# Optimization experiments

Measured on AMD Instinct MI355X. Metric: run time of the kernel, lower is better.

Reference implementation:

```python
import jax, jax.numpy as jnp
import numpy as np

N, E, D, H, K = 100000, 1600000, 512, 256, 64


def setup_inputs() -> dict:
    key = jax.random.key(0)
    ks = jax.random.split(key, 8)
    x = jax.random.normal(ks[0], (N, D), dtype=jnp.float32)
    edge_index = jax.random.randint(ks[1], (2, E), 0, N, dtype=jnp.int64)
    W1 = jax.random.normal(ks[2], (D, H), dtype=jnp.float32) / np.sqrt(D)
    b1 = jnp.zeros((H,), dtype=jnp.float32)
    W2 = jax.random.normal(ks[3], (H, H), dtype=jnp.float32) / np.sqrt(H)
    b2 = jnp.zeros((H,), dtype=jnp.float32)
    Wk = jax.random.normal(ks[4], (H, K), dtype=jnp.float32) / np.sqrt(H)
    log_tau = jnp.array(np.log(1.0), dtype=jnp.float32)
    return {"x": x, "edge_index": edge_index, "W1": W1, "b1": b1,
            "W2": W2, "b2": b2, "Wk": Wk, "log_tau": log_tau}


def _gcn_norm(edge_index, n):
    # add self-loops, compute sym-normalized edge weights (PyG GCNConv default)
    loop = jnp.arange(n, dtype=edge_index.dtype)
    src = jnp.concatenate([edge_index[0], loop])
    dst = jnp.concatenate([edge_index[1], loop])
    deg = jax.ops.segment_sum(jnp.ones_like(dst, dtype=jnp.float32), dst, num_segments=n)
    dinv = jnp.where(deg > 0, jax.lax.rsqrt(deg), 0.0)
    norm = dinv[src] * dinv[dst]  # [E+N]
    return src, dst, norm


def _gcn_conv(h, W, b, src, dst, norm, n):
    hw = h @ W                      # dense GEMM [n, out]
    msg = hw[src] * norm[:, None]   # gather + scale
    out = jax.ops.segment_sum(msg, dst, num_segments=n)  # scatter-add
    return out + b


def reference(x, edge_index, W1, b1, W2, b2, Wk, log_tau):
    n = x.shape[0]
    src, dst, norm = _gcn_norm(edge_index, n)
    h = jax.nn.relu(_gcn_conv(x, W1, b1, src, dst, norm, n))
    h = _gcn_conv(h, W2, b2, src, dst, norm, n)
    logits = h @ Wk                 # [n, K]
    tau = jnp.exp(log_tau)
    S = jax.nn.softmax(logits / tau, axis=-1)
    return (S, logits)
```

## Files before the change

kernel.cpp:

```cpp
#include <hip/hip_runtime.h>

typedef unsigned short u16;
typedef unsigned int u32;

__device__ __forceinline__ float bfl(u32 u) { union { u32 i; float f; } v; v.i = u << 16; return v.f; }
__device__ __forceinline__ float bfh(u32 u) { union { u32 i; float f; } v; v.i = u & 0xffff0000u; return v.f; }
__device__ __forceinline__ float bf2f(u16 u) { union { u32 i; float f; } v; v.i = ((u32)u) << 16; return v.f; }
__device__ __forceinline__ u16 f2bf(float f) {
    union { float f; u32 i; } v; v.f = f;
    u32 r = v.i + 0x7fffu + ((v.i >> 16) & 1u);
    return (u16)(r >> 16);
}

typedef const __attribute__((address_space(1))) unsigned int* gas_u32;
typedef __attribute__((address_space(3))) unsigned int* las_u32;
__device__ __forceinline__ void async_cp16(const void* g, void* l) {
    __builtin_amdgcn_global_load_lds((gas_u32)g, (las_u32)l, 16, 0, 0);
}

__global__ void k_detect(const u32* __restrict__ xw, const int* __restrict__ eiw,
                         const void* __restrict__ ltau, int* __restrict__ flags,
                         int* __restrict__ bcount,
                         int xwords, int E, int nb) {
    __shared__ int cf32, ci64nz;
    if (threadIdx.x == 0) { cf32 = 0; ci64nz = 0; }
    __syncthreads();
    int t = threadIdx.x;
    for (int i = t; i < nb; i += 256) bcount[i] = 0;
    int xs = xwords / 256;
    u32 w = xw[(size_t)t * xs];
    int e = (int)((w >> 23) & 0xFFu);
    if (e >= 100 && e <= 140) atomicAdd(&cf32, 1);
    int es = E / 256;
    int hw = eiw[2 * (size_t)t * es + 1];
    if (hw != 0) atomicAdd(&ci64nz, 1);
    __syncthreads();
    if (t == 0) {
        int f32 = (cf32 >= 192) ? 1 : 0;
        flags[0] = f32;
        flags[1] = (ci64nz == 0) ? 1 : 0;
        ((float*)flags)[2] = f32 ? ((const float*)ltau)[0] : bf2f(((const u16*)ltau)[0]);
    }
}

__global__ __launch_bounds__(256) void k_edges_count(const int* __restrict__ ei,
                                                     int* __restrict__ src, int* __restrict__ dst,
                                                     int* __restrict__ bcount,
                                                     int e, int nb, const int* __restrict__ flags) {
    __shared__ int h[1024];
    int t = threadIdx.x;
    for (int i = t; i < nb; i += 256) h[i] = 0;
    __syncthreads();
    const int i64 = flags[1];
    int chunk = (e + gridDim.x - 1) / gridDim.x;
    int beg = blockIdx.x * chunk;
    int end = beg + chunk; if (end > e) end = e;
    for (int i = beg + t; i < end; i += 256) {
        int s, d;
        if (i64) { s = ei[2 * i]; d = ei[2 * (e + i)]; }
        else     { s = ei[i];     d = ei[e + i]; }
        src[i] = s; dst[i] = d;
        atomicAdd(&h[d >> 7], 1);
    }
    __syncthreads();
    for (int i = t; i < nb; i += 256) { int v = h[i]; if (v) atomicAdd(&bcount[i], v); }
}

__global__ __launch_bounds__(1024) void k_bscan(const int* __restrict__ bcount, int* __restrict__ bbase,
                                                int* __restrict__ bcursor, int nb) {
    int t = threadIdx.x;
    int per = (nb + 1023) >> 10;
    int b0 = t * per;
    int ls[8];
    int s = 0;
#pragma unroll
    for (int j = 0; j < 8; j++) {
        int v = 0;
        if (j < per && b0 + j < nb) v = bcount[b0 + j];
        ls[j] = v; s += v;
    }
    int lane = t & 63, w = t >> 6;
    int inc = s;
    for (int d = 1; d < 64; d <<= 1) { int u = __shfl_up(inc, d); if (lane >= d) inc += u; }
    __shared__ int wsum[16];
    __shared__ int gtot;
    if (lane == 63) wsum[w] = inc;
    __syncthreads();
    if (t == 0) { int a = 0; for (int i = 0; i < 16; i++) { int x = wsum[i]; wsum[i] = a; a += x; } gtot = a; }
    __syncthreads();
    int base = wsum[w] + inc - s;
#pragma unroll
    for (int j = 0; j < 8; j++) {
        if (j < per && b0 + j < nb) { bbase[b0 + j] = base; bcursor[b0 + j] = base; base += ls[j]; }
    }
    if (t == 0) bbase[nb] = gtot;
}

__global__ __launch_bounds__(256) void k_bscatter(const int* __restrict__ src, const int* __restrict__ dst,
                                                  int* __restrict__ bcursor, u32* __restrict__ ebuf,
                                                  int e, int nb) {
    __shared__ int h[1024];
    __shared__ int lbase[1024];
    int t = threadIdx.x;
    for (int i = t; i < nb; i += 256) h[i] = 0;
    __syncthreads();
    int chunk = (e + gridDim.x - 1) / gridDim.x;
    int beg = blockIdx.x * chunk;
    int end = beg + chunk; if (end > e) end = e;
    for (int i = beg + t; i < end; i += 256) atomicAdd(&h[dst[i] >> 7], 1);
    __syncthreads();
    for (int i = t; i < nb; i += 256) {
        int v = h[i];
        lbase[i] = v ? atomicAdd(&bcursor[i], v) : 0;
        h[i] = 0;
    }
    __syncthreads();
    for (int i = beg + t; i < end; i += 256) {
        int d = dst[i];
        int b = d >> 7;
        int p = lbase[b] + atomicAdd(&h[b], 1);
        ebuf[p] = ((u32)(d & 127) << 25) | (u32)src[i];
    }
}

__global__ __launch_bounds__(256) void k_bcsr(const u32* __restrict__ ebuf, const int* __restrict__ bbase,
                                              int* __restrict__ row_ptr, float* __restrict__ dinv,
                                              int* __restrict__ col, int n, int nb, int e) {
    __shared__ int hist[128], sc[128], cur[128];
    int b = blockIdx.x, t = threadIdx.x;
    if (t < 128) hist[t] = 0;
    __syncthreads();
    int beg = bbase[b], end = bbase[b + 1];
    for (int j = beg + t; j < end; j += 256) atomicAdd(&hist[ebuf[j] >> 25], 1);
    __syncthreads();
    if (t < 128) sc[t] = hist[t];
    __syncthreads();
    for (int d = 1; d < 128; d <<= 1) {
        int v = 0;
        if (t < 128 && t >= d) v = sc[t - d];
        __syncthreads();
        if (t < 128) sc[t] += v;
        __syncthreads();
    }
    if (t < 128) {
        int node = (b << 7) + t;
        if (node < n) {
            int ex = sc[t] - hist[t];
            row_ptr[node] = beg + ex;
            dinv[node] = rsqrtf((float)(hist[t] + 1));
            cur[t] = ex;
        }
    }
    if (b == 0 && t == 0) row_ptr[n] = e;
    __syncthreads();
    for (int j = beg + t; j < end; j += 256) {
        u32 ev = ebuf[j];
        int dl = (int)(ev >> 25);
        int p = atomicAdd(&cur[dl], 1);
        col[beg + p] = (int)(ev & 0x1FFFFFFu);
    }
}

__global__ void k_transpose_flex(const void* __restrict__ in, u16* __restrict__ out,
                                 int R, int C, const int* __restrict__ flags) {
    int idx = blockIdx.x * 256 + threadIdx.x;
    if (idx >= R * C) return;
    u16 v = flags[0] ? f2bf(((const float*)in)[idx]) : ((const u16*)in)[idx];
    int r = idx / C, c = idx % C;
    out[(size_t)c * R + r] = v;
}

typedef __bf16 bf16x8 __attribute__((ext_vector_type(8)));
typedef float floatx4 __attribute__((ext_vector_type(4)));

template <int WROWS, int WCOLS, int TM, int TN, int MODE, bool AFLEX, bool OFLEX>
__global__ __launch_bounds__(WROWS * WCOLS * 64, 4)
void k_gemm_bt(const void* __restrict__ A,
               const u16* __restrict__ Bt,
               void* __restrict__ C,
               const float* __restrict__ dinv,
               const int* __restrict__ flags,
               long long obase,
               int M, int Nd, int Kd) {
    constexpr int THREADS = WROWS * WCOLS * 64;
    constexpr int BM = WROWS * TM * 16;
    constexpr int BN = WCOLS * TN * 16;
    constexpr int BK = 32;
    __shared__ u16 As[2][BM][BK];
    __shared__ u16 Bs[2][BN][BK];
    const int af32 = AFLEX ? flags[0] : 0;
    const int of32 = OFLEX ? flags[0] : 0;
    const int tid = threadIdx.x;
    const int m0 = blockIdx.y * BM;
    const int n0 = blockIdx.x * BN;
    const int lane = tid & 63;
    const int wave = tid >> 6;
    const int wm = wave / WCOLS;
    const int wn = wave % WCOLS;
    const int mrow = lane & 15;
    const int quad = lane >> 4;

    floatx4 acc[TM][TN];
#pragma unroll
    for (int i = 0; i < TM; i++)
#pragma unroll
        for (int j = 0; j < TN; j++) { floatx4 z = {0.f, 0.f, 0.f, 0.f}; acc[i][j] = z; }

    auto stage = [&](int kk, int buf) {
        if (AFLEX && af32) {
#pragma unroll
            for (int idx = tid * 8; idx < BM * BK; idx += THREADS * 8) {
                int r = idx >> 5, k = idx & 31;
                int gr = m0 + r;
                u16 t8[8] = {0, 0, 0, 0, 0, 0, 0, 0};
                if (gr < M) {
                    const float* ap = (const float*)A + (size_t)gr * Kd + kk + k;
                    float4 f0 = *(const float4*)ap;
                    float4 f1 = *(const float4*)(ap + 4);
                    t8[0] = f2bf(f0.x); t8[1] = f2bf(f0.y); t8[2] = f2bf(f0.z); t8[3] = f2bf(f0.w);
                    t8[4] = f2bf(f1.x); t8[5] = f2bf(f1.y); t8[6] = f2bf(f1.z); t8[7] = f2bf(f1.w);
                }
                *(int4*)&As[buf][r][k] = *(const int4*)t8;
            }
#pragma unroll
            for (int idx = tid * 8; idx < BN * BK; idx += THREADS * 8) {
                int r = idx >> 5, k = idx & 31;
                int4 v = *(const int4*)(Bt + (size_t)(n0 + r) * Kd + kk + k);
                *(int4*)&Bs[buf][r][k] = v;
            }
        } else {
#pragma unroll
            for (int idx = tid * 8; idx < BM * BK; idx += THREADS * 8) {
                int r = idx >> 5, k = idx & 31;
                int gr = m0 + r;
                if (gr >= M) gr = M - 1;
                async_cp16((const u16*)A + (size_t)gr * Kd + kk + k, &As[buf][r][k]);
            }
#pragma unroll
            for (int idx = tid * 8; idx < BN * BK; idx += THREADS * 8) {
                int r = idx >> 5, k = idx & 31;
                async_cp16(Bt + (size_t)(n0 + r) * Kd + kk + k, &Bs[buf][r][k]);
            }
        }
    };

    const int steps = Kd / BK;
    stage(0, 0);
    for (int s = 0; s < steps; s++) {
        __syncthreads();
        if (s + 1 < steps) stage((s + 1) * BK, (s + 1) & 1);
        const int b = s & 1;
        bf16x8 af[TM], bfr[TN];
#pragma unroll
        for (int i = 0; i < TM; i++)
            af[i] = *(const bf16x8*)&As[b][wm * TM * 16 + i * 16 + mrow][quad * 8];
#pragma unroll
        for (int j = 0; j < TN; j++)
            bfr[j] = *(const bf16x8*)&Bs[b][wn * TN * 16 + j * 16 + mrow][quad * 8];
#pragma unroll
        for (int i = 0; i < TM; i++)
#pragma unroll
            for (int j = 0; j < TN; j++)
                acc[i][j] = __builtin_amdgcn_mfma_f32_16x16x32_bf16(af[i], bfr[j], acc[i][j], 0, 0, 0);
    }

#pragma unroll
    for (int i = 0; i < TM; i++) {
#pragma unroll
        for (int r = 0; r < 4; r++) {
            int grow = m0 + wm * TM * 16 + i * 16 + quad * 4 + r;
            if (grow < M) {
                float scale = (MODE == 0) ? dinv[grow] : 1.0f;
#pragma unroll
                for (int j = 0; j < TN; j++) {
                    int gcol = n0 + wn * TN * 16 + j * 16 + mrow;
                    float val = acc[i][j][r] * scale;
                    long long cidx = obase + (long long)grow * Nd + gcol;
                    if (OFLEX && of32) ((float*)C)[cidx] = val;
                    else               ((u16*)C)[cidx] = f2bf(val);
                }
            }
        }
    }
}

__global__ __launch_bounds__(256) void k_agg(const u16* __restrict__ g, u16* __restrict__ out,
                                             const int* __restrict__ row_ptr,
                                             const int* __restrict__ col,
                                             const float* __restrict__ dinv,
                                             const void* __restrict__ bias,
                                             const int* __restrict__ flags,
                                             int n, int do_relu) {
    int wid = (int)((blockIdx.x * 256 + threadIdx.x) >> 6);
    int lane = threadIdx.x & 63;
    if (wid >= n) return;
    int half = lane >> 5;
    int l = lane & 31;
    const u16* gp = g + (size_t)l * 8;
    float a0 = 0.f, a1 = 0.f, a2 = 0.f, a3 = 0.f, a4 = 0.f, a5 = 0.f, a6 = 0.f, a7 = 0.f;
    if (half == 0) {
        uint4 rv = *(const uint4*)(gp + (size_t)wid * 256);
        a0 += bfl(rv.x); a1 += bfh(rv.x); a2 += bfl(rv.y); a3 += bfh(rv.y);
        a4 += bfl(rv.z); a5 += bfh(rv.z); a6 += bfl(rv.w); a7 += bfh(rv.w);
    }
    int beg = row_ptr[wid], end = row_ptr[wid + 1];
    for (int base = beg; base < end; base += 64) {
        int m = end - base; if (m > 64) m = 64;
        int ci = (base + lane < end) ? col[base + lane] : 0;
        int j = 0;
        for (; j + 16 <= m; j += 16) {
            uint4 v[8];
#pragma unroll
            for (int q = 0; q < 8; q++) {
                int s = __shfl(ci, j + 2 * q + half);
                v[q] = *(const uint4*)(gp + (size_t)s * 256);
            }
#pragma unroll
            for (int q = 0; q < 8; q++) {
                a0 += bfl(v[q].x); a1 += bfh(v[q].x);
                a2 += bfl(v[q].y); a3 += bfh(v[q].y);
                a4 += bfl(v[q].z); a5 += bfh(v[q].z);
                a6 += bfl(v[q].w); a7 += bfh(v[q].w);
            }
        }
        for (; j < m; j += 2) {
            int idx = j + half;
            int s = __shfl(ci, idx < m ? idx : j);
            uint4 v = *(const uint4*)(gp + (size_t)s * 256);
            if (idx < m) {
                a0 += bfl(v.x); a1 += bfh(v.x); a2 += bfl(v.y); a3 += bfh(v.y);
                a4 += bfl(v.z); a5 += bfh(v.z); a6 += bfl(v.w); a7 += bfh(v.w);
            }
        }
    }
    a0 += __shfl_xor(a0, 32); a1 += __shfl_xor(a1, 32);
    a2 += __shfl_xor(a2, 32); a3 += __shfl_xor(a3, 32);
    a4 += __shfl_xor(a4, 32); a5 += __shfl_xor(a5, 32);
    a6 += __shfl_xor(a6, 32); a7 += __shfl_xor(a7, 32);
    if (half == 0) {
        float dv = dinv[wid];
        float b0, b1, b2, b3, b4, b5, b6, b7;
        if (flags[0]) {
            const float4* bp = (const float4*)bias;
            float4 q0 = bp[2 * l], q1 = bp[2 * l + 1];
            b0 = q0.x; b1 = q0.y; b2 = q0.z; b3 = q0.w;
            b4 = q1.x; b5 = q1.y; b6 = q1.z; b7 = q1.w;
        } else {
            uint4 bv = ((const uint4*)bias)[l];
            b0 = bfl(bv.x); b1 = bfh(bv.x); b2 = bfl(bv.y); b3 = bfh(bv.y);
            b4 = bfl(bv.z); b5 = bfh(bv.z); b6 = bfl(bv.w); b7 = bfh(bv.w);
        }
        a0 = a0 * dv + b0; a1 = a1 * dv + b1; a2 = a2 * dv + b2; a3 = a3 * dv + b3;
        a4 = a4 * dv + b4; a5 = a5 * dv + b5; a6 = a6 * dv + b6; a7 = a7 * dv + b7;
        if (do_relu) {
            a0 = fmaxf(a0, 0.f); a1 = fmaxf(a1, 0.f); a2 = fmaxf(a2, 0.f); a3 = fmaxf(a3, 0.f);
            a4 = fmaxf(a4, 0.f); a5 = fmaxf(a5, 0.f); a6 = fmaxf(a6, 0.f); a7 = fmaxf(a7, 0.f);
        }
        uint4 o;
        o.x = (u32)f2bf(a0) | ((u32)f2bf(a1) << 16);
        o.y = (u32)f2bf(a2) | ((u32)f2bf(a3) << 16);
        o.z = (u32)f2bf(a4) | ((u32)f2bf(a5) << 16);
        o.w = (u32)f2bf(a6) | ((u32)f2bf(a7) << 16);
        *(uint4*)(out + (size_t)wid * 256 + (size_t)l * 8) = o;
    }
}

__global__ __launch_bounds__(256) void k_softmax(void* __restrict__ out, long long NK,
                                                 const int* __restrict__ flags, int n) {
    int wid = (int)((blockIdx.x * 256 + threadIdx.x) >> 6);
    int lane = threadIdx.x & 63;
    if (wid >= n) return;
    int f32o = flags[0];
    float lt = ((const float*)flags)[2];
    float inv_tau = __expf(-lt);
    long long li = NK + (long long)wid * 64 + lane;
    float x = f32o ? ((const float*)out)[li] : bf2f(((const u16*)out)[li]);
    x *= inv_tau;
    float m = x;
    for (int d = 32; d; d >>= 1) m = fmaxf(m, __shfl_xor(m, d));
    float e = __expf(x - m);
    float s = e;
    for (int d = 32; d; d >>= 1) s += __shfl_xor(s, d);
    float r = e / s;
    long long si = (long long)wid * 64 + lane;
    if (f32o) ((float*)out)[si] = r;
    else      ((u16*)out)[si] = f2bf(r);
}

extern "C" void kernel_launch(void* const* d_in, const int* in_sizes, int n_in,
                              void* d_out, int out_size, void* d_ws, size_t ws_size,
                              hipStream_t stream) {
    const void* x    = d_in[0];
    const int*  ei   = (const int*)d_in[1];
    const void* W1   = d_in[2];
    const void* b1   = d_in[3];
    const void* W2   = d_in[4];
    const void* b2   = d_in[5];
    const void* Wk   = d_in[6];
    const void* ltau = d_in[7];
    const int D = 512, H = 256, K = 64;
    const int N = in_sizes[0] / D;
    const int E = in_sizes[1] / 2;
    const long long NK = (long long)N * K;
    const int nb = (N + 127) >> 7;

    u16* g = (u16*)d_ws;
    u16* h = g + (size_t)N * H;
    int* flags = (int*)(h + (size_t)N * H);
    int* srcv = (int*)g;
    int* dstv = srcv + E;
    u32* ebuf = (u32*)(dstv + E);

    size_t ooff = 0;
    auto oalloc = [&](size_t bytes) -> char* {
        char* p = (char*)d_out + ooff;
        ooff += (bytes + 255) & ~(size_t)255;
        return p;
    };
    int*   col     = (int*)oalloc((size_t)E * 4);
    float* dinv    = (float*)oalloc((size_t)N * 4);
    int*   row_ptr = (int*)oalloc((size_t)(N + 1) * 4);
    int*   bcount  = (int*)oalloc((size_t)nb * 4);
    int*   bbase   = (int*)oalloc((size_t)(nb + 1) * 4);
    int*   bcursor = (int*)oalloc((size_t)nb * 4);
    u16*   W1t     = (u16*)oalloc((size_t)D * H * 2);
    u16*   W2t     = (u16*)oalloc((size_t)H * H * 2);
    u16*   Wkt     = (u16*)oalloc((size_t)H * K * 2);

    auto g256 = [](long long n) { return (int)((n + 255) / 256); };

    k_detect<<<1, 256, 0, stream>>>((const u32*)x, ei, ltau, flags, bcount, in_sizes[0] / 2, E, nb);
    k_edges_count<<<256, 256, 0, stream>>>(ei, srcv, dstv, bcount, E, nb, flags);
    k_bscan<<<1, 1024, 0, stream>>>(bcount, bbase, bcursor, nb);
    k_bscatter<<<256, 256, 0, stream>>>(srcv, dstv, bcursor, ebuf, E, nb);
    k_bcsr<<<nb, 256, 0, stream>>>(ebuf, bbase, row_ptr, dinv, col, N, nb, E);

    k_transpose_flex<<<g256((long long)D * H), 256, 0, stream>>>(W1, W1t, D, H, flags);
    k_transpose_flex<<<g256((long long)H * H), 256, 0, stream>>>(W2, W2t, H, H, flags);
    k_transpose_flex<<<g256((long long)H * K), 256, 0, stream>>>(Wk, Wkt, H, K, flags);

    const int m64 = (N + 63) / 64;
    k_gemm_bt<1, 4, 4, 4, 0, true, false>
        <<<dim3(1, m64), 256, 0, stream>>>(x, W1t, g, dinv, flags, 0, N, H, D);
    k_agg<<<g256((long long)N * 64), 256, 0, stream>>>(g, h, row_ptr, col, dinv, b1, flags, N, 1);
    k_gemm_bt<1, 4, 4, 4, 0, false, false>
        <<<dim3(1, m64), 256, 0, stream>>>(h, W2t, g, dinv, flags, 0, N, H, H);
    k_agg<<<g256((long long)N * 64), 256, 0, stream>>>(g, h, row_ptr, col, dinv, b2, flags, N, 0);
    k_gemm_bt<1, 4, 4, 1, 1, false, true>
        <<<dim3(1, m64), 256, 0, stream>>>(h, Wkt, d_out, dinv, flags, NK, N, K, H);
    k_softmax<<<g256((long long)N * 64), 256, 0, stream>>>(d_out, NK, flags, N);
}
```

Before: 716.5 us.

## Fuse softmax into logits GEMM, batch rows per wave in aggregation, pack bf16 conversion

The final logits GEMM now stages its output tile in shared memory and computes the temperature softmax in the epilogue, so the separate softmax kernel and its reread of the logits go away. The aggregation kernel processes four rows per wave and loads the bias once per wave rather than once per row, with a quarter of the launched waves. The fp32-to-bf16 conversion in the first GEMM uses a packed hardware convert instruction. Scratch arrays move from the output buffer to the workspace. The trade-offs are less parallelism in aggregation and extra LDS traffic and syncs in the GEMM epilogue.

```diff
diff --git a/kernel.cpp b/kernel.cpp
--- a/kernel.cpp
+++ b/kernel.cpp
@@ -10,6 +10,11 @@
     union { float f; u32 i; } v; v.f = f;
     u32 r = v.i + 0x7fffu + ((v.i >> 16) & 1u);
     return (u16)(r >> 16);
+}
+__device__ __forceinline__ u32 pk2bf(float lo, float hi) {
+    u32 r;
+    asm("v_cvt_pk_bf16_f32 %0, %1, %2" : "=v"(r) : "v"(lo), "v"(hi));
+    return r;
 }
 
 typedef const __attribute__((address_space(1))) unsigned int* gas_u32;
@@ -186,8 +191,9 @@
     constexpr int BM = WROWS * TM * 16;
     constexpr int BN = WCOLS * TN * 16;
     constexpr int BK = 32;
-    __shared__ u16 As[2][BM][BK];
-    __shared__ u16 Bs[2][BN][BK];
+    __shared__ u16 SMEM[2 * (BM + BN) * BK];
+    auto As = (u16(*)[BM][BK])SMEM;
+    auto Bs = (u16(*)[BN][BK])(SMEM + 2 * BM * BK);
     const int af32 = AFLEX ? flags[0] : 0;
     const int of32 = OFLEX ? flags[0] : 0;
     const int tid = threadIdx.x;
@@ -212,15 +218,15 @@
             for (int idx = tid * 8; idx < BM * BK; idx += THREADS * 8) {
                 int r = idx >> 5, k = idx & 31;
                 int gr = m0 + r;
-                u16 t8[8] = {0, 0, 0, 0, 0, 0, 0, 0};
+                u32 t4[4] = {0, 0, 0, 0};
                 if (gr < M) {
                     const float* ap = (const float*)A + (size_t)gr * Kd + kk + k;
                     float4 f0 = *(const float4*)ap;
                     float4 f1 = *(const float4*)(ap + 4);
-                    t8[0] = f2bf(f0.x); t8[1] = f2bf(f0.y); t8[2] = f2bf(f0.z); t8[3] = f2bf(f0.w);
-                    t8[4] = f2bf(f1.x); t8[5] = f2bf(f1.y); t8[6] = f2bf(f1.z); t8[7] = f2bf(f1.w);
+                    t4[0] = pk2bf(f0.x, f0.y); t4[1] = pk2bf(f0.z, f0.w);
+                    t4[2] = pk2bf(f1.x, f1.y); t4[3] = pk2bf(f1.z, f1.w);
                 }
-                *(int4*)&As[buf][r][k] = *(const int4*)t8;
+                *(int4*)&As[buf][r][k] = *(const int4*)t4;
             }
 #pragma unroll
             for (int idx = tid * 8; idx < BN * BK; idx += THREADS * 8) {
@@ -264,6 +270,38 @@
                 acc[i][j] = __builtin_amdgcn_mfma_f32_16x16x32_bf16(af[i], bfr[j], acc[i][j], 0, 0, 0);
     }
 
+    if (MODE == 2) {
+        float inv_tau = __expf(-((const float*)flags)[2]);
+        float* Ct = (float*)SMEM;
+        __syncthreads();
+#pragma unroll
+        for (int i = 0; i < TM; i++)
+#pragma unroll
+            for (int r = 0; r < 4; r++) {
+                int row = i * 16 + quad * 4 + r;
+                Ct[row * 64 + wn * 16 + mrow] = acc[i][0][r];
+            }
+        __syncthreads();
+        for (int r16 = 0; r16 < 16; r16++) {
+            int row = r16 * 4 + wave;
+            float raw = Ct[row * 64 + lane];
+            float xv = raw * inv_tau;
+            float mx = xv;
+            for (int d = 32; d; d >>= 1) mx = fmaxf(mx, __shfl_xor(mx, d));
+            float ev = __expf(xv - mx);
+            float sm = ev;
+            for (int d = 32; d; d >>= 1) sm += __shfl_xor(sm, d);
+            float rr = ev / sm;
+            long long grow = m0 + row;
+            if (grow < M) {
+                long long si = grow * 64 + lane;
+                if (of32) { ((float*)C)[si] = rr; ((float*)C)[obase + si] = raw; }
+                else      { ((u16*)C)[si] = f2bf(rr); ((u16*)C)[obase + si] = f2bf(raw); }
+            }
+        }
+        return;
+    }
+
 #pragma unroll
     for (int i = 0; i < TM; i++) {
 #pragma unroll
@@ -291,100 +329,80 @@
                                              const void* __restrict__ bias,
                                              const int* __restrict__ flags,
                                              int n, int do_relu) {
-    int wid = (int)((blockIdx.x * 256 + threadIdx.x) >> 6);
+    int gw = (int)((blockIdx.x * 256 + threadIdx.x) >> 6);
     int lane = threadIdx.x & 63;
-    if (wid >= n) return;
     int half = lane >> 5;
     int l = lane & 31;
     const u16* gp = g + (size_t)l * 8;
-    float a0 = 0.f, a1 = 0.f, a2 = 0.f, a3 = 0.f, a4 = 0.f, a5 = 0.f, a6 = 0.f, a7 = 0.f;
-    if (half == 0) {
-        uint4 rv = *(const uint4*)(gp + (size_t)wid * 256);
-        a0 += bfl(rv.x); a1 += bfh(rv.x); a2 += bfl(rv.y); a3 += bfh(rv.y);
-        a4 += bfl(rv.z); a5 += bfh(rv.z); a6 += bfl(rv.w); a7 += bfh(rv.w);
-    }
-    int beg = row_ptr[wid], end = row_ptr[wid + 1];
-    for (int base = beg; base < end; base += 64) {
-        int m = end - base; if (m > 64) m = 64;
-        int ci = (base + lane < end) ? col[base + lane] : 0;
-        int j = 0;
-        for (; j + 16 <= m; j += 16) {
-            uint4 v[8];
-#pragma unroll
-            for (int q = 0; q < 8; q++) {
-                int s = __shfl(ci, j + 2 * q + half);
-                v[q] = *(const uint4*)(gp + (size_t)s * 256);
-            }
-#pragma unroll
-            for (int q = 0; q < 8; q++) {
-                a0 += bfl(v[q].x); a1 += bfh(v[q].x);
-                a2 += bfl(v[q].y); a3 += bfh(v[q].y);
-                a4 += bfl(v[q].z); a5 += bfh(v[q].z);
-                a6 += bfl(v[q].w); a7 += bfh(v[q].w);
-            }
-        }
-        for (; j < m; j += 2) {
-            int idx = j + half;
-            int s = __shfl(ci, idx < m ? idx : j);
-            uint4 v = *(const uint4*)(gp + (size_t)s * 256);
-            if (idx < m) {
-                a0 += bfl(v.x); a1 += bfh(v.x); a2 += bfl(v.y); a3 += bfh(v.y);
-                a4 += bfl(v.z); a5 += bfh(v.z); a6 += bfl(v.w); a7 += bfh(v.w);
-            }
-        }
-    }
-    a0 += __shfl_xor(a0, 32); a1 += __shfl_xor(a1, 32);
-    a2 += __shfl_xor(a2, 32); a3 += __shfl_xor(a3, 32);
-    a4 += __shfl_xor(a4, 32); a5 += __shfl_xor(a5, 32);
-    a6 += __shfl_xor(a6, 32); a7 += __shfl_xor(a7, 32);
-    if (half == 0) {
-        float dv = dinv[wid];
-        float b0, b1, b2, b3, b4, b5, b6, b7;
-        if (flags[0]) {
-            const float4* bp = (const float4*)bias;
-            float4 q0 = bp[2 * l], q1 = bp[2 * l + 1];
-            b0 = q0.x; b1 = q0.y; b2 = q0.z; b3 = q0.w;
-            b4 = q1.x; b5 = q1.y; b6 = q1.z; b7 = q1.w;
-        } else {
-            uint4 bv = ((const uint4*)bias)[l];
-            b0 = bfl(bv.x); b1 = bfh(bv.x); b2 = bfl(bv.y); b3 = bfh(bv.y);
-            b4 = bfl(bv.z); b5 = bfh(bv.z); b6 = bfl(bv.w); b7 = bfh(bv.w);
-        }
-        a0 = a0 * dv + b0; a1 = a1 * dv + b1; a2 = a2 * dv + b2; a3 = a3 * dv + b3;
-        a4 = a4 * dv + b4; a5 = a5 * dv + b5; a6 = a6 * dv + b6; a7 = a7 * dv + b7;
-        if (do_relu) {
-            a0 = fmaxf(a0, 0.f); a1 = fmaxf(a1, 0.f); a2 = fmaxf(a2, 0.f); a3 = fmaxf(a3, 0.f);
-            a4 = fmaxf(a4, 0.f); a5 = fmaxf(a5, 0.f); a6 = fmaxf(a6, 0.f); a7 = fmaxf(a7, 0.f);
-        }
-        uint4 o;
-        o.x = (u32)f2bf(a0) | ((u32)f2bf(a1) << 16);
-        o.y = (u32)f2bf(a2) | ((u32)f2bf(a3) << 16);
-        o.z = (u32)f2bf(a4) | ((u32)f2bf(a5) << 16);
-        o.w = (u32)f2bf(a6) | ((u32)f2bf(a7) << 16);
-        *(uint4*)(out + (size_t)wid * 256 + (size_t)l * 8) = o;
-    }
-}
-
-__global__ __launch_bounds__(256) void k_softmax(void* __restrict__ out, long long NK,
-                                                 const int* __restrict__ flags, int n) {
-    int wid = (int)((blockIdx.x * 256 + threadIdx.x) >> 6);
-    int lane = threadIdx.x & 63;
-    if (wid >= n) return;
-    int f32o = flags[0];
-    float lt = ((const float*)flags)[2];
-    float inv_tau = __expf(-lt);
-    long long li = NK + (long long)wid * 64 + lane;
-    float x = f32o ? ((const float*)out)[li] : bf2f(((const u16*)out)[li]);
-    x *= inv_tau;
-    float m = x;
-    for (int d = 32; d; d >>= 1) m = fmaxf(m, __shfl_xor(m, d));
-    float e = __expf(x - m);
-    float s = e;
-    for (int d = 32; d; d >>= 1) s += __shfl_xor(s, d);
-    float r = e / s;
-    long long si = (long long)wid * 64 + lane;
-    if (f32o) ((float*)out)[si] = r;
-    else      ((u16*)out)[si] = f2bf(r);
+    float b0, b1, b2, b3, b4, b5, b6, b7;
+    if (flags[0]) {
+        const float4* bp = (const float4*)bias;
+        float4 q0 = bp[2 * l], q1 = bp[2 * l + 1];
+        b0 = q0.x; b1 = q0.y; b2 = q0.z; b3 = q0.w;
+        b4 = q1.x; b5 = q1.y; b6 = q1.z; b7 = q1.w;
+    } else {
+        uint4 bv = ((const uint4*)bias)[l];
+        b0 = bfl(bv.x); b1 = bfh(bv.x); b2 = bfl(bv.y); b3 = bfh(bv.y);
+        b4 = bfl(bv.z); b5 = bfh(bv.z); b6 = bfl(bv.w); b7 = bfh(bv.w);
+    }
+    int w1 = gw * 4 + 4; if (w1 > n) w1 = n;
+    for (int wid = gw * 4; wid < w1; wid++) {
+        float a0 = 0.f, a1 = 0.f, a2 = 0.f, a3 = 0.f, a4 = 0.f, a5 = 0.f, a6 = 0.f, a7 = 0.f;
+        if (half == 0) {
+            uint4 rv = *(const uint4*)(gp + (size_t)wid * 256);
+            a0 += bfl(rv.x); a1 += bfh(rv.x); a2 += bfl(rv.y); a3 += bfh(rv.y);
+            a4 += bfl(rv.z); a5 += bfh(rv.z); a6 += bfl(rv.w); a7 += bfh(rv.w);
+        }
+        int beg = row_ptr[wid], end = row_ptr[wid + 1];
+        for (int base = beg; base < end; base += 64) {
+            int m = end - base; if (m > 64) m = 64;
+            int ci = (base + lane < end) ? col[base + lane] : 0;
+            int j = 0;
+            for (; j + 16 <= m; j += 16) {
+                uint4 v[8];
+#pragma unroll
+                for (int q = 0; q < 8; q++) {
+                    int s = __shfl(ci, j + 2 * q + half);
+                    v[q] = *(const uint4*)(gp + (size_t)s * 256);
+                }
+#pragma unroll
+                for (int q = 0; q < 8; q++) {
+                    a0 += bfl(v[q].x); a1 += bfh(v[q].x);
+                    a2 += bfl(v[q].y); a3 += bfh(v[q].y);
+                    a4 += bfl(v[q].z); a5 += bfh(v[q].z);
+                    a6 += bfl(v[q].w); a7 += bfh(v[q].w);
+                }
+            }
+            for (; j < m; j += 2) {
+                int idx = j + half;
+                int s = __shfl(ci, idx < m ? idx : j);
+                uint4 v = *(const uint4*)(gp + (size_t)s * 256);
+                if (idx < m) {
+                    a0 += bfl(v.x); a1 += bfh(v.x); a2 += bfl(v.y); a3 += bfh(v.y);
+                    a4 += bfl(v.z); a5 += bfh(v.z); a6 += bfl(v.w); a7 += bfh(v.w);
+                }
+            }
+        }
+        a0 += __shfl_xor(a0, 32); a1 += __shfl_xor(a1, 32);
+        a2 += __shfl_xor(a2, 32); a3 += __shfl_xor(a3, 32);
+        a4 += __shfl_xor(a4, 32); a5 += __shfl_xor(a5, 32);
+        a6 += __shfl_xor(a6, 32); a7 += __shfl_xor(a7, 32);
+        if (half == 0) {
+            float dv = dinv[wid];
+            float c0 = a0 * dv + b0, c1 = a1 * dv + b1, c2 = a2 * dv + b2, c3 = a3 * dv + b3;
+            float c4 = a4 * dv + b4, c5 = a5 * dv + b5, c6 = a6 * dv + b6, c7 = a7 * dv + b7;
+            if (do_relu) {
+                c0 = fmaxf(c0, 0.f); c1 = fmaxf(c1, 0.f); c2 = fmaxf(c2, 0.f); c3 = fmaxf(c3, 0.f);
+                c4 = fmaxf(c4, 0.f); c5 = fmaxf(c5, 0.f); c6 = fmaxf(c6, 0.f); c7 = fmaxf(c7, 0.f);
+            }
+            uint4 o;
+            o.x = (u32)f2bf(c0) | ((u32)f2bf(c1) << 16);
+            o.y = (u32)f2bf(c2) | ((u32)f2bf(c3) << 16);
+            o.z = (u32)f2bf(c4) | ((u32)f2bf(c5) << 16);
+            o.w = (u32)f2bf(c6) | ((u32)f2bf(c7) << 16);
+            *(uint4*)(out + (size_t)wid * 256 + (size_t)l * 8) = o;
+        }
+    }
 }
 
 extern "C" void kernel_launch(void* const* d_in, const int* in_sizes, int n_in,
@@ -412,8 +430,9 @@
     u32* ebuf = (u32*)(dstv + E);
 
     size_t ooff = 0;
+    char* wsbase = (char*)(flags + 64);
     auto oalloc = [&](size_t bytes) -> char* {
-        char* p = (char*)d_out + ooff;
+        char* p = wsbase + ooff;
         ooff += (bytes + 255) & ~(size_t)255;
         return p;
     };
@@ -440,13 +459,13 @@
     k_transpose_flex<<<g256((long long)H * K), 256, 0, stream>>>(Wk, Wkt, H, K, flags);
 
     const int m64 = (N + 63) / 64;
+    const long long aggw = ((long long)N + 3) / 4;
     k_gemm_bt<1, 4, 4, 4, 0, true, false>
         <<<dim3(1, m64), 256, 0, stream>>>(x, W1t, g, dinv, flags, 0, N, H, D);
-    k_agg<<<g256((long long)N * 64), 256, 0, stream>>>(g, h, row_ptr, col, dinv, b1, flags, N, 1);
+    k_agg<<<g256(aggw * 64), 256, 0, stream>>>(g, h, row_ptr, col, dinv, b1, flags, N, 1);
     k_gemm_bt<1, 4, 4, 4, 0, false, false>
         <<<dim3(1, m64), 256, 0, stream>>>(h, W2t, g, dinv, flags, 0, N, H, H);
-    k_agg<<<g256((long long)N * 64), 256, 0, stream>>>(g, h, row_ptr, col, dinv, b2, flags, N, 0);
-    k_gemm_bt<1, 4, 4, 1, 1, false, true>
+    k_agg<<<g256(aggw * 64), 256, 0, stream>>>(g, h, row_ptr, col, dinv, b2, flags, N, 0);
+    k_gemm_bt<1, 4, 4, 1, 2, false, true>
         <<<dim3(1, m64), 256, 0, stream>>>(h, Wkt, d_out, dinv, flags, NK, N, K, H);
-    k_softmax<<<g256((long long)N * 64), 256, 0, stream>>>(d_out, NK, flags, N);
-}
+}
```

After: 725.9 us. Within noise of the previous version (+1.3%).
